# Optimization experiments

Measured on AMD Instinct MI355X. Metric: run time of the kernel, lower is better.

Reference implementation:

```python
import jax, jax.numpy as jnp
import numpy as np


def setup_inputs() -> dict:
    key = jax.random.key(0)
    k1, k2, k3, k4 = jax.random.split(key, 4)
    B, L, C, F = 64, 4096, 256, 128
    t = jax.random.uniform(k1, (B, L), dtype=jnp.float32)
    freqs = jax.random.normal(k2, (F,), dtype=jnp.float32)
    amp_sin = jax.random.normal(k3, (C, F), dtype=jnp.float32)
    amp_cos = jax.random.normal(k4, (C, F), dtype=jnp.float32)
    return {"t": t, "freqs": freqs, "amp_sin": amp_sin, "amp_cos": amp_cos}


def reference(t, freqs, amp_sin, amp_cos):
    # angles: (B, L, F) = 2*pi * freqs * t  (broadcast over last dim)
    angles = (2.0 * jnp.pi) * t[..., None] * freqs  # (B, L, F)
    # sum over frequencies with per-channel amplitudes is a GEMM:
    # out[b,l,c] = sum_f sin(angles)[b,l,f]*amp_sin[c,f] + cos(angles)[b,l,f]*amp_cos[c,f]
    out = jnp.einsum('blf,cf->blc', jnp.sin(angles), amp_sin)
    out = out + jnp.einsum('blf,cf->blc', jnp.cos(angles), amp_cos)
    return out  # (B, L, C)
```

## Files before the change

### kernel.cpp

```cpp
#include <hip/hip_runtime.h>
#include <stdint.h>


typedef __bf16 bf16x8 __attribute__((ext_vector_type(8)));
typedef float  floatx4 __attribute__((ext_vector_type(4)));

#define MT    64
#define F_    128
#define C_    256
#define LSTR  264
#define TPB   8

#define LDS_BARRIER() asm volatile("s_waitcnt lgkmcnt(0)\n\ts_barrier" ::: "memory")

__global__ __launch_bounds__(256, 2)
void fourier_fused(const float* __restrict__ t,
                   const float* __restrict__ freqs,
                   const float* __restrict__ amp_sin,
                   const float* __restrict__ amp_cos,
                   float* __restrict__ out)
{
    __shared__ __align__(16) __bf16 Af[2][MT * LSTR];

    const int tid  = threadIdx.x;
    const int wave = tid >> 6;
    const int lane = tid & 63;
    const int l15  = lane & 15;
    const int quad = lane >> 4;
    const int n0   = wave * 64;

    const int fgrp = tid & 15;
    const int rsub = tid >> 4;

    const int tile0 = blockIdx.x * TPB;

    float tv[4];
    #pragma unroll
    for (int p = 0; p < 4; ++p)
        tv[p] = t[tile0 * MT + p * 16 + rsub];

    const float4 f0v = *(const float4*)(freqs + fgrp * 8);
    const float4 f1v = *(const float4*)(freqs + fgrp * 8 + 4);
    const float fr[8] = {f0v.x, f0v.y, f0v.z, f0v.w, f1v.x, f1v.y, f1v.z, f1v.w};

    bf16x8 b[8][4];
    #pragma unroll
    for (int ks = 0; ks < 8; ++ks) {
        const float* __restrict__ amp = (ks < 4) ? amp_sin : amp_cos;
        const int f0 = (ks & 3) * 32 + quad * 8;
        #pragma unroll
        for (int ni = 0; ni < 4; ++ni) {
            const float* p = amp + (n0 + ni * 16 + l15) * F_ + f0;
            const float4 b0 = *(const float4*)(p);
            const float4 b1 = *(const float4*)(p + 4);
            b[ks][ni][0] = (__bf16)b0.x; b[ks][ni][1] = (__bf16)b0.y;
            b[ks][ni][2] = (__bf16)b0.z; b[ks][ni][3] = (__bf16)b0.w;
            b[ks][ni][4] = (__bf16)b1.x; b[ks][ni][5] = (__bf16)b1.y;
            b[ks][ni][6] = (__bf16)b1.z; b[ks][ni][7] = (__bf16)b1.w;
        }
    }

    #pragma unroll 2
    for (int it = 0; it < TPB; ++it) {
        const int m0 = (tile0 + it) * MT;
        __bf16* __restrict__ A = Af[it & 1];

        float tvn[4];
        {
            const int mb = (it + 1 < TPB) ? (m0 + MT) : tile0 * MT;
            #pragma unroll
            for (int p = 0; p < 4; ++p)
                tvn[p] = t[mb + p * 16 + rsub];
        }

        #pragma unroll
        for (int pass = 0; pass < 4; ++pass) {
            const int ml = pass * 16 + rsub;
            const float tval = tv[pass];
            bf16x8 sv, cv;
            #pragma unroll
            for (int j = 0; j < 8; ++j) {
                const float r = __builtin_amdgcn_fractf(tval * fr[j]);
                sv[j] = (__bf16)__builtin_amdgcn_sinf(r);
                cv[j] = (__bf16)__builtin_amdgcn_cosf(r);
            }
            *(bf16x8*)&A[ml * LSTR + fgrp * 8]      = sv;
            *(bf16x8*)&A[ml * LSTR + F_ + fgrp * 8] = cv;
        }
        LDS_BARRIER();

        floatx4 acc[4][4];
        #pragma unroll
        for (int mi = 0; mi < 4; ++mi)
            #pragma unroll
            for (int ni = 0; ni < 4; ++ni)
                acc[mi][ni] = (floatx4){0.f, 0.f, 0.f, 0.f};

        #pragma unroll
        for (int ks = 0; ks < 8; ++ks) {
            const int ak = ks * 32 + quad * 8;
            bf16x8 a[4];
            #pragma unroll
            for (int mi = 0; mi < 4; ++mi)
                a[mi] = *(const bf16x8*)&A[(mi * 16 + l15) * LSTR + ak];
            #pragma unroll
            for (int mi = 0; mi < 4; ++mi)
                #pragma unroll
                for (int ni = 0; ni < 4; ++ni)
                    acc[mi][ni] = __builtin_amdgcn_mfma_f32_16x16x32_bf16(
                        a[mi], b[ks][ni], acc[mi][ni], 0, 0, 0);
        }

        #pragma unroll
        for (int mi = 0; mi < 4; ++mi) {
            #pragma unroll
            for (int r = 0; r < 4; ++r) {
                const int m = m0 + mi * 16 + quad * 4 + r;
                float* row = out + (size_t)m * C_ + n0 + l15;
                #pragma unroll
                for (int ni = 0; ni < 4; ++ni)
                    row[ni * 16] = acc[mi][ni][r];
            }
        }

        #pragma unroll
        for (int p = 0; p < 4; ++p) tv[p] = tvn[p];
    }
}

extern "C" void kernel_launch(void* const* d_in, const int* in_sizes, int n_in,
                              void* d_out, int out_size, void* d_ws, size_t ws_size,
                              hipStream_t stream) {
    const float* t   = (const float*)d_in[0];
    const float* fq  = (const float*)d_in[1];
    const float* As  = (const float*)d_in[2];
    const float* Ac  = (const float*)d_in[3];
    float* outp      = (float*)d_out;

    const int M = in_sizes[0];
    hipLaunchKernelGGL(fourier_fused, dim3(M / (MT * TPB)), dim3(256), 0, stream,
                       t, fq, As, Ac, outp);
}
```

Before: 277.8 us.

## Split channels across blocks, shrink M tile, and swap MFMA operands for vector stores

Halves the row tile to 32 and splits the 256 output channels across two blocks of 128, so each wave holds fewer B fragments and accumulators. The launch bound rises to 4 blocks per CU and the grid doubles. MFMA operands are swapped so each lane holds four consecutive channels, letting the epilogue write one float4 per fragment instead of scattered scalar stores. In exchange, every sin/cos value is now computed twice (once per channel block), and the amplitude loads are duplicated across more blocks.

```diff
diff --git a/kernel.cpp b/kernel.cpp
--- a/kernel.cpp
+++ b/kernel.cpp
@@ -5,15 +5,16 @@
 typedef __bf16 bf16x8 __attribute__((ext_vector_type(8)));
 typedef float  floatx4 __attribute__((ext_vector_type(4)));
 
-#define MT    64
+#define MT    32
 #define F_    128
 #define C_    256
+#define CB    128
 #define LSTR  264
 #define TPB   8
 
 #define LDS_BARRIER() asm volatile("s_waitcnt lgkmcnt(0)\n\ts_barrier" ::: "memory")
 
-__global__ __launch_bounds__(256, 2)
+__global__ __launch_bounds__(256, 4)
 void fourier_fused(const float* __restrict__ t,
                    const float* __restrict__ freqs,
                    const float* __restrict__ amp_sin,
@@ -27,29 +28,31 @@
     const int lane = tid & 63;
     const int l15  = lane & 15;
     const int quad = lane >> 4;
-    const int n0   = wave * 64;
+
+    const int cblk = blockIdx.x & 1;
+    const int mblk = blockIdx.x >> 1;
+    const int n0   = cblk * CB + wave * 32;
 
     const int fgrp = tid & 15;
     const int rsub = tid >> 4;
 
-    const int tile0 = blockIdx.x * TPB;
+    const int tile0 = mblk * TPB;
 
-    float tv[4];
-    #pragma unroll
-    for (int p = 0; p < 4; ++p)
-        tv[p] = t[tile0 * MT + p * 16 + rsub];
+    float tv[2];
+    tv[0] = t[tile0 * MT + rsub];
+    tv[1] = t[tile0 * MT + 16 + rsub];
 
     const float4 f0v = *(const float4*)(freqs + fgrp * 8);
     const float4 f1v = *(const float4*)(freqs + fgrp * 8 + 4);
     const float fr[8] = {f0v.x, f0v.y, f0v.z, f0v.w, f1v.x, f1v.y, f1v.z, f1v.w};
 
-    bf16x8 b[8][4];
+    bf16x8 b[8][2];
     #pragma unroll
     for (int ks = 0; ks < 8; ++ks) {
         const float* __restrict__ amp = (ks < 4) ? amp_sin : amp_cos;
         const int f0 = (ks & 3) * 32 + quad * 8;
         #pragma unroll
-        for (int ni = 0; ni < 4; ++ni) {
+        for (int ni = 0; ni < 2; ++ni) {
             const float* p = amp + (n0 + ni * 16 + l15) * F_ + f0;
             const float4 b0 = *(const float4*)(p);
             const float4 b1 = *(const float4*)(p + 4);
@@ -65,16 +68,15 @@
         const int m0 = (tile0 + it) * MT;
         __bf16* __restrict__ A = Af[it & 1];
 
-        float tvn[4];
+        float tvn[2];
         {
             const int mb = (it + 1 < TPB) ? (m0 + MT) : tile0 * MT;
-            #pragma unroll
-            for (int p = 0; p < 4; ++p)
-                tvn[p] = t[mb + p * 16 + rsub];
+            tvn[0] = t[mb + rsub];
+            tvn[1] = t[mb + 16 + rsub];
         }
 
         #pragma unroll
-        for (int pass = 0; pass < 4; ++pass) {
+        for (int pass = 0; pass < 2; ++pass) {
             const int ml = pass * 16 + rsub;
             const float tval = tv[pass];
             bf16x8 sv, cv;
@@ -89,42 +91,40 @@
         }
         LDS_BARRIER();
 
-        floatx4 acc[4][4];
+        floatx4 acc[2][2];
         #pragma unroll
-        for (int mi = 0; mi < 4; ++mi)
+        for (int mi = 0; mi < 2; ++mi)
             #pragma unroll
-            for (int ni = 0; ni < 4; ++ni)
+            for (int ni = 0; ni < 2; ++ni)
                 acc[mi][ni] = (floatx4){0.f, 0.f, 0.f, 0.f};
 
         #pragma unroll
         for (int ks = 0; ks < 8; ++ks) {
             const int ak = ks * 32 + quad * 8;
-            bf16x8 a[4];
+            bf16x8 a[2];
             #pragma unroll
-            for (int mi = 0; mi < 4; ++mi)
+            for (int mi = 0; mi < 2; ++mi)
                 a[mi] = *(const bf16x8*)&A[(mi * 16 + l15) * LSTR + ak];
             #pragma unroll
-            for (int mi = 0; mi < 4; ++mi)
+            for (int mi = 0; mi < 2; ++mi)
                 #pragma unroll
-                for (int ni = 0; ni < 4; ++ni)
+                for (int ni = 0; ni < 2; ++ni)
                     acc[mi][ni] = __builtin_amdgcn_mfma_f32_16x16x32_bf16(
-                        a[mi], b[ks][ni], acc[mi][ni], 0, 0, 0);
+                        b[ks][ni], a[mi], acc[mi][ni], 0, 0, 0);
         }
 
         #pragma unroll
-        for (int mi = 0; mi < 4; ++mi) {
+        for (int mi = 0; mi < 2; ++mi) {
             #pragma unroll
-            for (int r = 0; r < 4; ++r) {
-                const int m = m0 + mi * 16 + quad * 4 + r;
-                float* row = out + (size_t)m * C_ + n0 + l15;
-                #pragma unroll
-                for (int ni = 0; ni < 4; ++ni)
-                    row[ni * 16] = acc[mi][ni][r];
+            for (int ni = 0; ni < 2; ++ni) {
+                float* p = out + (size_t)(m0 + mi * 16 + l15) * C_
+                               + n0 + ni * 16 + quad * 4;
+                *(floatx4*)p = acc[mi][ni];
             }
         }
 
-        #pragma unroll
-        for (int p = 0; p < 4; ++p) tv[p] = tvn[p];
+        tv[0] = tvn[0];
+        tv[1] = tvn[1];
     }
 }
 
@@ -138,6 +138,6 @@
     float* outp      = (float*)d_out;
 
     const int M = in_sizes[0];
-    hipLaunchKernelGGL(fourier_fused, dim3(M / (MT * TPB)), dim3(256), 0, stream,
-                       t, fq, As, Ac, outp);
+    hipLaunchKernelGGL(fourier_fused, dim3((M / (MT * TPB)) * 2), dim3(256), 0,
+                       stream, t, fq, As, Ac, outp);
 }
```

Result: slower. 300.8 us (+8.3%).
